# Kernel tuning notes

Hardware: AMD Instinct MI355X
Metric: run time of the kernel (lower is better)

The kernel has to match this reference:

```python
import jax, jax.numpy as jnp
import numpy as np

D = 1024
H = 16
HD = D // H
FF = 4 * D

def layer_norm(x, g, b, eps=1e-5):
    mu = jnp.mean(x, axis=-1, keepdims=True)
    var = jnp.var(x, axis=-1, keepdims=True)
    return (x - mu) * jax.lax.rsqrt(var + eps) * g + b

def setup_inputs() -> dict:
    key = jax.random.key(0)
    ks = jax.random.split(key, 8)
    s = 0.02
    return {
        "x": jax.random.normal(ks[0], (2, 2048, D), jnp.float32),
        "ln1_g": jnp.ones((D,), jnp.float32),
        "ln1_b": jnp.zeros((D,), jnp.float32),
        "w_qkv": jax.random.normal(ks[1], (3 * D, D), jnp.float32) * s,
        "b_qkv": jnp.zeros((3 * D,), jnp.float32),
        "w_proj": jax.random.normal(ks[2], (D, D), jnp.float32) * s,
        "b_proj": jnp.zeros((D,), jnp.float32),
        "ln2_g": jnp.ones((D,), jnp.float32),
        "ln2_b": jnp.zeros((D,), jnp.float32),
        "w_fc1": jax.random.normal(ks[3], (FF, D), jnp.float32) * s,
        "b_fc1": jnp.zeros((FF,), jnp.float32),
        "w_fc2": jax.random.normal(ks[4], (D, FF), jnp.float32) * s,
        "b_fc2": jnp.zeros((D,), jnp.float32),
    }

def reference(x, ln1_g, ln1_b, w_qkv, b_qkv, w_proj, b_proj,
              ln2_g, ln2_b, w_fc1, b_fc1, w_fc2, b_fc2):
    B, N, C = x.shape
    scale = HD ** -0.5
    # --- attention branch (pre-norm) ---
    h = layer_norm(x, ln1_g, ln1_b)
    qkv = h @ w_qkv.T + b_qkv                      # [B,N,3D]
    qkv = qkv.reshape(B, N, 3, H, HD).transpose(2, 0, 3, 1, 4)
    q, k, v = qkv[0], qkv[1], qkv[2]               # [B,H,N,HD]
    attn = jnp.einsum('bhnd,bhmd->bhnm', q, k) * scale
    attn = jax.nn.softmax(attn, axis=-1)
    o = jnp.einsum('bhnm,bhmd->bhnd', attn, v)     # [B,H,N,HD]
    o = o.transpose(0, 2, 1, 3).reshape(B, N, C)
    x = x + (o @ w_proj.T + b_proj)
    # --- FFN branch (pre-norm) ---
    h = layer_norm(x, ln2_g, ln2_b)
    h = jax.nn.gelu(h @ w_fc1.T + b_fc1, approximate=False)
    x = x + (h @ w_fc2.T + b_fc2)
    return x
```

## Files before the change

### kernel.cpp

```cpp
#include <hip/hip_runtime.h>

typedef __attribute__((ext_vector_type(8))) short short8;
typedef __attribute__((ext_vector_type(4))) float f32x4;

static __device__ __forceinline__ unsigned short f2bf(float f){
  unsigned u = __float_as_uint(f);
  u += 0x7FFF + ((u >> 16) & 1);
  return (unsigned short)(u >> 16);
}

static __device__ __forceinline__ f32x4 MF(short8 a, short8 b, f32x4 c){
  return __builtin_amdgcn_mfma_f32_16x16x32_bf16(a, b, c, 0, 0, 0);
}

#define GL16(g, l) __builtin_amdgcn_global_load_lds( \
    (const __attribute__((address_space(1))) void*)(g), \
    (__attribute__((address_space(3))) void*)(l), 16, 0, 0)

#define SBAR { __builtin_amdgcn_sched_barrier(0); __builtin_amdgcn_s_barrier(); __builtin_amdgcn_sched_barrier(0); }

__global__ __launch_bounds__(256) void cvt_all(
    const float* __restrict__ a0, const float* __restrict__ a1,
    const float* __restrict__ a2, const float* __restrict__ a3,
    unsigned short* __restrict__ o0, unsigned short* __restrict__ o1,
    unsigned short* __restrict__ o2, unsigned short* __restrict__ o3){
  int i = blockIdx.x * 256 + threadIdx.x;
  const float* src; unsigned short* dst; int off;
  if (i < 786432)       { src = a0; dst = o0; off = i; }
  else if (i < 1048576) { src = a1; dst = o1; off = i - 786432; }
  else if (i < 2097152) { src = a2; dst = o2; off = i - 1048576; }
  else                  { src = a3; dst = o3; off = i - 2097152; }
  float4 v = reinterpret_cast<const float4*>(src)[off];
  ushort4 o;
  o.x = f2bf(v.x); o.y = f2bf(v.y); o.z = f2bf(v.z); o.w = f2bf(v.w);
  reinterpret_cast<ushort4*>(dst)[off] = o;
}

__global__ __launch_bounds__(256) void ln_bf16(const float* __restrict__ x,
    const float* __restrict__ g, const float* __restrict__ b,
    unsigned short* __restrict__ out){
  int row = blockIdx.x, t = threadIdx.x;
  const float* xr = x + (size_t)row * 1024;
  float4 xv = reinterpret_cast<const float4*>(xr)[t];
  float s  = xv.x + xv.y + xv.z + xv.w;
  float sq = xv.x*xv.x + xv.y*xv.y + xv.z*xv.z + xv.w*xv.w;
  #pragma unroll
  for (int m = 32; m >= 1; m >>= 1){ s += __shfl_xor(s, m); sq += __shfl_xor(sq, m); }
  __shared__ float ss[4], ssq[4];
  int w = t >> 6, lane = t & 63;
  if (lane == 0){ ss[w] = s; ssq[w] = sq; }
  __syncthreads();
  s  = ss[0] + ss[1] + ss[2] + ss[3];
  sq = ssq[0] + ssq[1] + ssq[2] + ssq[3];
  float mu = s * (1.f/1024.f);
  float rs = rsqrtf(sq * (1.f/1024.f) - mu*mu + 1e-5f);
  float4 gv = reinterpret_cast<const float4*>(g)[t];
  float4 bv = reinterpret_cast<const float4*>(b)[t];
  ushort4 o;
  o.x = f2bf((xv.x - mu) * rs * gv.x + bv.x);
  o.y = f2bf((xv.y - mu) * rs * gv.y + bv.y);
  o.z = f2bf((xv.z - mu) * rs * gv.z + bv.z);
  o.w = f2bf((xv.w - mu) * rs * gv.w + bv.w);
  reinterpret_cast<ushort4*>(out + (size_t)row * 1024)[t] = o;
}

template<int EPI>
__global__ __launch_bounds__(512, 2) void gemm8p(
    const unsigned short* __restrict__ A,
    const unsigned short* __restrict__ B,
    const float* __restrict__ bias,
    void* __restrict__ C,
    int M, int N, int K)
{
  __shared__ __attribute__((aligned(16))) short As[2 * 256 * 64];
  __shared__ __attribute__((aligned(16))) short Bs[2 * 256 * 64];
  const int NT = K >> 6;
  int tid = threadIdx.x, lane = tid & 63, wave = tid >> 6;
  int wm = wave >> 2, wn = wave & 3;
  int l15 = lane & 15, hi = lane >> 4;
  int hi2 = hi ^ (((l15 >> 2) & 1) << 1);
  int bm = blockIdx.y * 256, bn = blockIdx.x * 256;
  int lr = lane >> 3;
  int sg8 = ((lane & 7) ^ ((lane >> 5) << 1)) * 8;
  int rb0 = wave * 16;

  f32x4 acc[8][4] = {};
  short8 aR[4][2], bA[2][2], bB[2][2];

  auto stage = [&](int T, int h){
    if (T >= NT) return;
    const unsigned short* src = (h < 2) ? (A + (size_t)(bm + ((h & 1) << 7)) * K)
                                        : (B + (size_t)(bn + ((h & 1) << 7)) * K);
    short* dst = ((h < 2) ? As : Bs) + ((T & 1) << 14) + ((h & 1) << 13);
    const unsigned short* s = src + (size_t)(rb0 + lr) * K + (T << 6) + sg8;
    GL16(s, dst + rb0 * 64);
    GL16(s + (size_t)8 * K, dst + (rb0 + 8) * 64);
  };
  auto LDA = [&](const short* Ab, int m, int kk){
    int R = wm * 128 + m * 16 + l15;
    return *(const short8*)(Ab + R * 64 + kk * 32 + hi2 * 8);
  };
  auto LDB = [&](const short* Bb, int n, int kk){
    int R = wn * 64 + n * 16 + l15;
    return *(const short8*)(Bb + R * 64 + kk * 32 + hi2 * 8);
  };

  stage(0, 0); stage(0, 1); stage(0, 2); stage(0, 3);
  stage(1, 0); stage(1, 1);
  asm volatile("s_waitcnt vmcnt(4)" ::: "memory");
  SBAR;

  for (int i = 0; i < (NT >> 1); ++i){
    int t0 = 2 * i, t1 = t0 + 1;
    const short* A0 = As;            const short* B0 = Bs;
    const short* A1 = As + 16384;    const short* B1 = Bs + 16384;
    #pragma unroll
    for (int m = 0; m < 4; m++){ aR[m][0] = LDA(A0, m, 0); aR[m][1] = LDA(A0, m, 1); }
    #pragma unroll
    for (int n = 0; n < 2; n++){ bA[n][0] = LDB(B0, n, 0); bA[n][1] = LDB(B0, n, 1); }
    __builtin_amdgcn_sched_barrier(0);
    stage(t1, 2);
    SBAR;
    __builtin_amdgcn_s_setprio(1);
    #pragma unroll
    for (int m = 0; m < 4; m++)
      #pragma unroll
      for (int n = 0; n < 2; n++)
        #pragma unroll
        for (int kk = 0; kk < 2; kk++) acc[m][n] = MF(aR[m][kk], bA[n][kk], acc[m][n]);
    __builtin_amdgcn_s_setprio(0);
    SBAR;
    #pragma unroll
    for (int n = 0; n < 2; n++){ bB[n][0] = LDB(B0, n + 2, 0); bB[n][1] = LDB(B0, n + 2, 1); }
    __builtin_amdgcn_sched_barrier(0);
    stage(t1, 3);
    SBAR;
    __builtin_amdgcn_s_setprio(1);
    #pragma unroll
    for (int m = 0; m < 4; m++)
      #pragma unroll
      for (int n = 0; n < 2; n++)
        #pragma unroll
        for (int kk = 0; kk < 2; kk++) acc[m][n + 2] = MF(aR[m][kk], bB[n][kk], acc[m][n + 2]);
    __builtin_amdgcn_s_setprio(0);
    SBAR;
    #pragma unroll
    for (int m = 0; m < 4; m++){ aR[m][0] = LDA(A0, m + 4, 0); aR[m][1] = LDA(A0, m + 4, 1); }
    __builtin_amdgcn_sched_barrier(0);
    stage(t0 + 2, 0);
    SBAR;
    __builtin_amdgcn_s_setprio(1);
    #pragma unroll
    for (int m = 0; m < 4; m++)
      #pragma unroll
      for (int n = 0; n < 2; n++)
        #pragma unroll
        for (int kk = 0; kk < 2; kk++) acc[m + 4][n] = MF(aR[m][kk], bA[n][kk], acc[m + 4][n]);
    __builtin_amdgcn_s_setprio(0);
    SBAR;
    stage(t0 + 2, 1);
    SBAR;
    __builtin_amdgcn_s_setprio(1);
    #pragma unroll
    for (int m = 0; m < 4; m++)
      #pragma unroll
      for (int n = 0; n < 2; n++)
        #pragma unroll
        for (int kk = 0; kk < 2; kk++) acc[m + 4][n + 2] = MF(aR[m][kk], bB[n][kk], acc[m + 4][n + 2]);
    __builtin_amdgcn_s_setprio(0);
    asm volatile("s_waitcnt vmcnt(4)" ::: "memory");
    SBAR;
    #pragma unroll
    for (int m = 0; m < 4; m++){ aR[m][0] = LDA(A1, m, 0); aR[m][1] = LDA(A1, m, 1); }
    #pragma unroll
    for (int n = 0; n < 2; n++){ bA[n][0] = LDB(B1, n, 0); bA[n][1] = LDB(B1, n, 1); }
    __builtin_amdgcn_sched_barrier(0);
    stage(t0 + 2, 2);
    SBAR;
    __builtin_amdgcn_s_setprio(1);
    #pragma unroll
    for (int m = 0; m < 4; m++)
      #pragma unroll
      for (int n = 0; n < 2; n++)
        #pragma unroll
        for (int kk = 0; kk < 2; kk++) acc[m][n] = MF(aR[m][kk], bA[n][kk], acc[m][n]);
    __builtin_amdgcn_s_setprio(0);
    SBAR;
    #pragma unroll
    for (int n = 0; n < 2; n++){ bB[n][0] = LDB(B1, n + 2, 0); bB[n][1] = LDB(B1, n + 2, 1); }
    __builtin_amdgcn_sched_barrier(0);
    stage(t0 + 2, 3);
    SBAR;
    __builtin_amdgcn_s_setprio(1);
    #pragma unroll
    for (int m = 0; m < 4; m++)
      #pragma unroll
      for (int n = 0; n < 2; n++)
        #pragma unroll
        for (int kk = 0; kk < 2; kk++) acc[m][n + 2] = MF(aR[m][kk], bB[n][kk], acc[m][n + 2]);
    __builtin_amdgcn_s_setprio(0);
    SBAR;
    #pragma unroll
    for (int m = 0; m < 4; m++){ aR[m][0] = LDA(A1, m + 4, 0); aR[m][1] = LDA(A1, m + 4, 1); }
    __builtin_amdgcn_sched_barrier(0);
    stage(t0 + 3, 0);
    SBAR;
    __builtin_amdgcn_s_setprio(1);
    #pragma unroll
    for (int m = 0; m < 4; m++)
      #pragma unroll
      for (int n = 0; n < 2; n++)
        #pragma unroll
        for (int kk = 0; kk < 2; kk++) acc[m + 4][n] = MF(aR[m][kk], bA[n][kk], acc[m + 4][n]);
    __builtin_amdgcn_s_setprio(0);
    SBAR;
    stage(t0 + 3, 1);
    SBAR;
    __builtin_amdgcn_s_setprio(1);
    #pragma unroll
    for (int m = 0; m < 4; m++)
      #pragma unroll
      for (int n = 0; n < 2; n++)
        #pragma unroll
        for (int kk = 0; kk < 2; kk++) acc[m + 4][n + 2] = MF(aR[m][kk], bB[n][kk], acc[m + 4][n + 2]);
    __builtin_amdgcn_s_setprio(0);
    asm volatile("s_waitcnt vmcnt(4)" ::: "memory");
    SBAR;
  }

  #pragma unroll
  for (int m = 0; m < 8; m++){
    int row = bm + wm * 128 + m * 16 + hi * 4;
    #pragma unroll
    for (int n = 0; n < 4; n++){
      int col = bn + wn * 64 + n * 16 + l15;
      float bv = bias[col];
      #pragma unroll
      for (int j = 0; j < 4; j++){
        float v = acc[m][n][j] + bv;
        if (EPI == 1){
          float w2 = v * v;
          float t = exp2f(v * fmaf(w2, 0.10294322f, 2.3022078f));
          float r = __builtin_amdgcn_rcpf(1.f + t);
          v = v - v * r;
        }
        ((unsigned short*)C)[(size_t)(row + j) * N + col] = f2bf(v);
      }
    }
  }
}

template<int EPI>
__global__ __launch_bounds__(512, 2) void gemm8p128(
    const unsigned short* __restrict__ A,
    const unsigned short* __restrict__ B,
    const float* __restrict__ bias,
    const float* __restrict__ resid,
    void* __restrict__ C,
    int M, int N, int K)
{
  __shared__ __attribute__((aligned(16))) short As[2][128 * 64];
  __shared__ __attribute__((aligned(16))) short Bs[2][128 * 64];
  const int NT = K >> 6;
  int tid = threadIdx.x, lane = tid & 63, wave = tid >> 6;
  int wm = wave >> 2, wn = wave & 3;
  int l15 = lane & 15, hi = lane >> 4, l7 = l15 & 7;
  int lin = blockIdx.y * 8 + blockIdx.x;
  int xcd = lin & 7, idx = lin >> 3;
  int bm = (xcd * 4 + (idx >> 3)) * 128;
  int bn = (idx & 7) * 128;
  int lr = lane >> 3;
  int sega = ((lane & 7) ^ lr) * 8;
  f32x4 acc[4][2] = {};
  short8 aR[4][2], bf0[2], bf1[2];

  auto stage = [&](int T, int h){
    if (T >= NT) return;
    const unsigned short* src = (h < 2) ? (A + (size_t)bm * K) : (B + (size_t)bn * K);
    short* dst = ((h < 2) ? &As[0][0] : &Bs[0][0]) + (T & 1) * (128 * 64);
    int row = ((h & 1) << 6) + wave * 8;
    GL16(src + (size_t)(row + lr) * K + (T << 6) + sega, dst + row * 64);
  };
  auto LDA = [&](const short* Ab, int m, int kk){
    int R = wm * 64 + m * 16 + l15;
    return *(const short8*)(Ab + R * 64 + (((kk << 2) | hi) ^ l7) * 8);
  };
  auto LDB = [&](const short* Bb, int n, int kk){
    int R = wn * 32 + n * 16 + l15;
    return *(const short8*)(Bb + R * 64 + (((kk << 2) | hi) ^ l7) * 8);
  };

  stage(0, 0); stage(0, 1); stage(0, 2); stage(0, 3);
  stage(1, 0); stage(1, 1);
  asm volatile("s_waitcnt vmcnt(2)" ::: "memory");
  SBAR;

  const short* A0 = &As[0][0]; const short* B0 = &Bs[0][0];
  const short* A1 = &As[1][0]; const short* B1 = &Bs[1][0];

  for (int i = 0; i < (NT >> 1) - 1; ++i){
    int t0 = 2 * i, t1 = t0 + 1;
    #pragma unroll
    for (int m = 0; m < 4; m++){ aR[m][0] = LDA(A0, m, 0); aR[m][1] = LDA(A0, m, 1); }
    bf0[0] = LDB(B0, 0, 0); bf0[1] = LDB(B0, 0, 1);
    __builtin_amdgcn_sched_barrier(0);
    stage(t1, 2); stage(t1, 3);
    SBAR;
    __builtin_amdgcn_s_setprio(1);
    #pragma unroll
    for (int m = 0; m < 4; m++)
      #pragma unroll
      for (int kk = 0; kk < 2; kk++) acc[m][0] = MF(aR[m][kk], bf0[kk], acc[m][0]);
    __builtin_amdgcn_s_setprio(0);
    SBAR;
    bf1[0] = LDB(B0, 1, 0); bf1[1] = LDB(B0, 1, 1);
    __builtin_amdgcn_sched_barrier(0);
    stage(t0 + 2, 0); stage(t0 + 2, 1);
    SBAR;
    __builtin_amdgcn_s_setprio(1);
    #pragma unroll
    for (int m = 0; m < 4; m++)
      #pragma unroll
      for (int kk = 0; kk < 2; kk++) acc[m][1] = MF(aR[m][kk], bf1[kk], acc[m][1]);
    __builtin_amdgcn_s_setprio(0);
    asm volatile("s_waitcnt vmcnt(2)" ::: "memory");
    SBAR;
    #pragma unroll
    for (int m = 0; m < 4; m++){ aR[m][0] = LDA(A1, m, 0); aR[m][1] = LDA(A1, m, 1); }
    bf0[0] = LDB(B1, 0, 0); bf0[1] = LDB(B1, 0, 1);
    __builtin_amdgcn_sched_barrier(0);
    stage(t0 + 2, 2); stage(t0 + 2, 3);
    SBAR;
    __builtin_amdgcn_s_setprio(1);
    #pragma unroll
    for (int m = 0; m < 4; m++)
      #pragma unroll
      for (int kk = 0; kk < 2; kk++) acc[m][0] = MF(aR[m][kk], bf0[kk], acc[m][0]);
    __builtin_amdgcn_s_setprio(0);
    SBAR;
    bf1[0] = LDB(B1, 1, 0); bf1[1] = LDB(B1, 1, 1);
    __builtin_amdgcn_sched_barrier(0);
    stage(t0 + 3, 0); stage(t0 + 3, 1);
    SBAR;
    __builtin_amdgcn_s_setprio(1);
    #pragma unroll
    for (int m = 0; m < 4; m++)
      #pragma unroll
      for (int kk = 0; kk < 2; kk++) acc[m][1] = MF(aR[m][kk], bf1[kk], acc[m][1]);
    __builtin_amdgcn_s_setprio(0);
    asm volatile("s_waitcnt vmcnt(2)" ::: "memory");
    SBAR;
  }
  {
    #pragma unroll
    for (int m = 0; m < 4; m++){ aR[m][0] = LDA(A0, m, 0); aR[m][1] = LDA(A0, m, 1); }
    bf0[0] = LDB(B0, 0, 0); bf0[1] = LDB(B0, 0, 1);
    __builtin_amdgcn_sched_barrier(0);
    int t1 = NT - 1;
    stage(t1, 2); stage(t1, 3);
    SBAR;
    __builtin_amdgcn_s_setprio(1);
    #pragma unroll
    for (int m = 0; m < 4; m++)
      #pragma unroll
      for (int kk = 0; kk < 2; kk++) acc[m][0] = MF(aR[m][kk], bf0[kk], acc[m][0]);
    __builtin_amdgcn_s_setprio(0);
    SBAR;
    bf1[0] = LDB(B0, 1, 0); bf1[1] = LDB(B0, 1, 1);
    SBAR;
    __builtin_amdgcn_s_setprio(1);
    #pragma unroll
    for (int m = 0; m < 4; m++)
      #pragma unroll
      for (int kk = 0; kk < 2; kk++) acc[m][1] = MF(aR[m][kk], bf1[kk], acc[m][1]);
    __builtin_amdgcn_s_setprio(0);
    asm volatile("s_waitcnt vmcnt(0)" ::: "memory");
    SBAR;
    #pragma unroll
    for (int m = 0; m < 4; m++){ aR[m][0] = LDA(A1, m, 0); aR[m][1] = LDA(A1, m, 1); }
    bf0[0] = LDB(B1, 0, 0); bf0[1] = LDB(B1, 0, 1);
    SBAR;
    __builtin_amdgcn_s_setprio(1);
    #pragma unroll
    for (int m = 0; m < 4; m++)
      #pragma unroll
      for (int kk = 0; kk < 2; kk++) acc[m][0] = MF(aR[m][kk], bf0[kk], acc[m][0]);
    __builtin_amdgcn_s_setprio(0);
    SBAR;
    bf1[0] = LDB(B1, 1, 0); bf1[1] = LDB(B1, 1, 1);
    __builtin_amdgcn_s_setprio(1);
    #pragma unroll
    for (int m = 0; m < 4; m++)
      #pragma unroll
      for (int kk = 0; kk < 2; kk++) acc[m][1] = MF(aR[m][kk], bf1[kk], acc[m][1]);
    __builtin_amdgcn_s_setprio(0);
  }

  #pragma unroll
  for (int m = 0; m < 4; m++){
    int row = bm + wm * 64 + m * 16 + hi * 4;
    #pragma unroll
    for (int n = 0; n < 2; n++){
      int col = bn + wn * 32 + n * 16 + l15;
      float bv = bias[col];
      #pragma unroll
      for (int j = 0; j < 4; j++){
        float v = acc[m][n][j] + bv;
        int r = row + j;
        if (EPI == 2){
          ((float*)C)[(size_t)r * N + col] = v + resid[(size_t)r * N + col];
        } else {
          ((unsigned short*)C)[(size_t)r * N + col] = f2bf(v);
        }
      }
    }
  }
}

__global__ __launch_bounds__(512) void attn_fwd(const unsigned short* __restrict__ qkv,
                                                unsigned short* __restrict__ o){
  __shared__ __attribute__((aligned(16))) short K_lds[2][64*64];
  __shared__ __attribute__((aligned(16))) short V_lds[2][64*64];
  __shared__ __attribute__((aligned(16))) short P_lds[8][16*64];
  int tid = threadIdx.x, wave = tid >> 6, lane = tid & 63;
  int l15 = lane & 15, hi = lane >> 4, l7 = l15 & 7;
  int bid = blockIdx.x;
  int swz = (bid & 7) * 64 + (bid >> 3);
  int qt = swz & 15, bh = swz >> 4;
  int b = bh >> 4, h = bh & 15;
  const unsigned short* qbase = qkv + (size_t)b * 2048 * 3072 + h * 64;
  const unsigned short* kbase = qbase + 1024;
  const unsigned short* vbase = qbase + 2048;
  int qrow = qt * 128 + wave * 16 + l15;
  short8 qf0 = *(const short8*)(qbase + (size_t)qrow * 3072 + hi * 8);
  short8 qf1 = *(const short8*)(qbase + (size_t)qrow * 3072 + 32 + hi * 8);
  #pragma unroll
  for (int j = 0; j < 8; j++){
    float q0 = __uint_as_float((unsigned)(unsigned short)qf0[j] << 16) * 0.18033688f;
    float q1 = __uint_as_float((unsigned)(unsigned short)qf1[j] << 16) * 0.18033688f;
    qf0[j] = (short)f2bf(q0);
    qf1[j] = (short)f2bf(q1);
  }
  short8 ones8;
  #pragma unroll
  for (int j = 0; j < 8; j++) ones8[j] = (short)0x3F80;
  int krow = tid >> 3, kseg = tid & 7;
  int vt = tid - 256;
  int kp = vt & 31, ds8 = (vt >> 5) & 7;
  int vcg = kp >> 2, vwi = (2 * kp) & 7;
  f32x4 accO[4] = {};
  f32x4 lacc = {};
  short* Pw = &P_lds[wave][0];

  {
    short8 kv = *(const short8*)(kbase + (size_t)krow * 3072 + kseg * 8);
    short8 vv0, vv1;
    if (vt >= 0){
      const unsigned short* vr = vbase + (size_t)(2 * kp) * 3072 + ds8 * 8;
      vv0 = *(const short8*)vr; vv1 = *(const short8*)(vr + 3072);
    }
    *(short8*)(&K_lds[0][krow * 64 + ((kseg ^ (krow & 7)) << 3)]) = kv;
    if (vt >= 0){
      unsigned* Vw = (unsigned*)&V_lds[0][0];
      #pragma unroll
      for (int j = 0; j < 8; j++){
        int d = ds8 * 8 + j;
        int sa = d * 64 + ((vcg ^ (d & 7)) << 3) + vwi;
        Vw[sa >> 1] = (unsigned)(unsigned short)vv0[j] | ((unsigned)(unsigned short)vv1[j] << 16);
      }
    }
    __syncthreads();
  }

  for (int t = 0; t < 32; t++){
    int cur = t & 1;
    const short* Kc = &K_lds[cur][0];
    const short* Vc = &V_lds[cur][0];
    short8 kv, vv0, vv1;
    if (t < 31){
      int kt = (t + 1) * 64;
      kv = *(const short8*)(kbase + (size_t)(kt + krow) * 3072 + kseg * 8);
      if (vt >= 0){
        const unsigned short* vr = vbase + (size_t)(kt + 2 * kp) * 3072 + ds8 * 8;
        vv0 = *(const short8*)vr; vv1 = *(const short8*)(vr + 3072);
      }
    }
    f32x4 sacc[4];
    __builtin_amdgcn_s_setprio(1);
    #pragma unroll
    for (int kb = 0; kb < 4; kb++){
      f32x4 s = {};
      short8 ka = *(const short8*)(Kc + (kb * 16 + l15) * 64 + ((hi ^ l7) << 3));
      s = __builtin_amdgcn_mfma_f32_16x16x32_bf16(ka, qf0, s, 0, 0, 0);
      short8 kb_ = *(const short8*)(Kc + (kb * 16 + l15) * 64 + (((4 + hi) ^ l7) << 3));
      s = __builtin_amdgcn_mfma_f32_16x16x32_bf16(kb_, qf1, s, 0, 0, 0);
      sacc[kb] = s;
    }
    __builtin_amdgcn_s_setprio(0);
    unsigned pu[8];
    #pragma unroll
    for (int kb = 0; kb < 4; kb++){
      unsigned u0 = (unsigned)(int)fmaf(sacc[kb][0], 128.f, 16248.6f);
      unsigned u1 = (unsigned)(int)fmaf(sacc[kb][1], 128.f, 16248.6f);
      unsigned u2 = (unsigned)(int)fmaf(sacc[kb][2], 128.f, 16248.6f);
      unsigned u3 = (unsigned)(int)fmaf(sacc[kb][3], 128.f, 16248.6f);
      pu[kb * 2]     = u0 | (u1 << 16);
      pu[kb * 2 + 1] = u2 | (u3 << 16);
    }
    #pragma unroll
    for (int kb = 0; kb < 4; kb++){
      int sa = l15 * 64 + ((((kb << 1) | (hi >> 1)) ^ l7) << 3) + ((hi & 1) << 2);
      *(uint2*)(Pw + sa) = make_uint2(pu[kb * 2], pu[kb * 2 + 1]);
    }
    __builtin_amdgcn_s_setprio(1);
    #pragma unroll
    for (int kb2 = 0; kb2 < 2; kb2++){
      short8 pf = *(const short8*)(Pw + l15 * 64 + ((((kb2 << 2) | hi) ^ l7) << 3));
      #pragma unroll
      for (int db = 0; db < 4; db++){
        short8 vf = *(const short8*)(Vc + (db * 16 + l15) * 64 + ((((kb2 << 2) | hi) ^ l7) << 3));
        accO[db] = __builtin_amdgcn_mfma_f32_16x16x32_bf16(vf, pf, accO[db], 0, 0, 0);
      }
      lacc = __builtin_amdgcn_mfma_f32_16x16x32_bf16(ones8, pf, lacc, 0, 0, 0);
    }
    __builtin_amdgcn_s_setprio(0);
    if (t < 31){
      int nxt = cur ^ 1;
      *(short8*)(&K_lds[nxt][krow * 64 + ((kseg ^ (krow & 7)) << 3)]) = kv;
      if (vt >= 0){
        unsigned* Vw = (unsigned*)&V_lds[nxt][0];
        #pragma unroll
        for (int j = 0; j < 8; j++){
          int d = ds8 * 8 + j;
          int sa = d * 64 + ((vcg ^ (d & 7)) << 3) + vwi;
          Vw[sa >> 1] = (unsigned)(unsigned short)vv0[j] | ((unsigned)(unsigned short)vv1[j] << 16);
        }
      }
      __syncthreads();
    }
  }
  float inv = 1.f / lacc[0];
  unsigned short* ob = o + (size_t)(b * 2048 + qt * 128 + wave * 16 + l15) * 1024 + h * 64;
  #pragma unroll
  for (int db = 0; db < 4; db++){
    ushort4 w;
    w.x = f2bf(accO[db][0] * inv);
    w.y = f2bf(accO[db][1] * inv);
    w.z = f2bf(accO[db][2] * inv);
    w.w = f2bf(accO[db][3] * inv);
    *(ushort4*)(ob + db * 16 + hi * 4) = w;
  }
}

extern "C" void kernel_launch(void* const* d_in, const int* in_sizes, int n_in,
                              void* d_out, int out_size, void* d_ws, size_t ws_size,
                              hipStream_t stream){
  const float* x      = (const float*)d_in[0];
  const float* ln1_g  = (const float*)d_in[1];
  const float* ln1_b  = (const float*)d_in[2];
  const float* w_qkv  = (const float*)d_in[3];
  const float* b_qkv  = (const float*)d_in[4];
  const float* w_proj = (const float*)d_in[5];
  const float* b_proj = (const float*)d_in[6];
  const float* ln2_g  = (const float*)d_in[7];
  const float* ln2_b  = (const float*)d_in[8];
  const float* w_fc1  = (const float*)d_in[9];
  const float* b_fc1  = (const float*)d_in[10];
  const float* w_fc2  = (const float*)d_in[11];
  const float* b_fc2  = (const float*)d_in[12];
  float* out = (float*)d_out;
  char* ws = (char*)d_ws;
  const size_t MB = 1024 * 1024;
  unsigned short* h     = (unsigned short*)(ws);
  unsigned short* qkv   = (unsigned short*)(ws + 8*MB);
  unsigned short* ob    = (unsigned short*)(ws + 32*MB);
  float*          x1    = (float*)(ws + 40*MB);
  unsigned short* f     = (unsigned short*)(ws + 56*MB);
  unsigned short* wqkvb = (unsigned short*)(ws + 88*MB);
  unsigned short* wprojb= (unsigned short*)(ws + 94*MB);
  unsigned short* wfc1b = (unsigned short*)(ws + 96*MB);
  unsigned short* wfc2b = (unsigned short*)(ws + 104*MB);

  cvt_all<<<12288, 256, 0, stream>>>(w_qkv, w_proj, w_fc1, w_fc2,
                                     wqkvb, wprojb, wfc1b, wfc2b);

  ln_bf16<<<4096, 256, 0, stream>>>(x, ln1_g, ln1_b, h);
  gemm8p<0><<<dim3(12, 16), 512, 0, stream>>>(h, wqkvb, b_qkv, qkv, 4096, 3072, 1024);
  attn_fwd<<<512, 512, 0, stream>>>(qkv, ob);
  gemm8p128<2><<<dim3(8, 32), 512, 0, stream>>>(ob, wprojb, b_proj, x, x1, 4096, 1024, 1024);
  ln_bf16<<<4096, 256, 0, stream>>>(x1, ln2_g, ln2_b, h);
  gemm8p<1><<<dim3(16, 16), 512, 0, stream>>>(h, wfc1b, b_fc1, f, 4096, 4096, 1024);
  gemm8p128<2><<<dim3(8, 32), 512, 0, stream>>>(f, wfc2b, b_fc2, x1, out, 4096, 1024, 4096);
}
```

Baseline: 221.8 us.

## Split K and V tile loading across wave halves and simplify GEMM block mapping

In the attention kernel, K-tile loading now goes to the first 256 threads, two 16-byte loads each, and V loading stays with the other 256 threads. Previously all 512 threads loaded K and half also loaded V. This balances per-thread global load and LDS store work and removes duplicated register pressure. The GEMM's XCD-aware block swizzle is also replaced with a plain row-major block mapping, which may change L2 locality across XCDs.

```diff
diff --git a/kernel.cpp b/kernel.cpp
--- a/kernel.cpp
+++ b/kernel.cpp
@@ -266,9 +266,8 @@
   int wm = wave >> 2, wn = wave & 3;
   int l15 = lane & 15, hi = lane >> 4, l7 = l15 & 7;
   int lin = blockIdx.y * 8 + blockIdx.x;
-  int xcd = lin & 7, idx = lin >> 3;
-  int bm = (xcd * 4 + (idx >> 3)) * 128;
-  int bn = (idx & 7) * 128;
+  int bn = (lin & 7) * 128;
+  int bm = (lin >> 3) * 128;
   int lr = lane >> 3;
   int sega = ((lane & 7) ^ lr) * 8;
   f32x4 acc[4][2] = {};
@@ -444,31 +443,45 @@
   short8 ones8;
   #pragma unroll
   for (int j = 0; j < 8; j++) ones8[j] = (short)0x3F80;
-  int krow = tid >> 3, kseg = tid & 7;
   int vt = tid - 256;
+  int ki0 = tid * 2, ki1 = ki0 + 1;
+  int kr0 = ki0 >> 3, ks0 = ki0 & 7;
+  int kr1 = ki1 >> 3, ks1 = ki1 & 7;
   int kp = vt & 31, ds8 = (vt >> 5) & 7;
   int vcg = kp >> 2, vwi = (2 * kp) & 7;
   f32x4 accO[4] = {};
   f32x4 lacc = {};
   short* Pw = &P_lds[wave][0];
 
-  {
-    short8 kv = *(const short8*)(kbase + (size_t)krow * 3072 + kseg * 8);
-    short8 vv0, vv1;
-    if (vt >= 0){
-      const unsigned short* vr = vbase + (size_t)(2 * kp) * 3072 + ds8 * 8;
-      vv0 = *(const short8*)vr; vv1 = *(const short8*)(vr + 3072);
-    }
-    *(short8*)(&K_lds[0][krow * 64 + ((kseg ^ (krow & 7)) << 3)]) = kv;
-    if (vt >= 0){
-      unsigned* Vw = (unsigned*)&V_lds[0][0];
+  auto kv_load = [&](int kt, short8& s0, short8& s1){
+    if (vt < 0){
+      s0 = *(const short8*)(kbase + (size_t)(kt + kr0) * 3072 + ks0 * 8);
+      s1 = *(const short8*)(kbase + (size_t)(kt + kr1) * 3072 + ks1 * 8);
+    } else {
+      const unsigned short* vr = vbase + (size_t)(kt + 2 * kp) * 3072 + ds8 * 8;
+      s0 = *(const short8*)vr;
+      s1 = *(const short8*)(vr + 3072);
+    }
+  };
+  auto kv_store = [&](int buf, short8 s0, short8 s1){
+    if (vt < 0){
+      *(short8*)(&K_lds[buf][kr0 * 64 + ((ks0 ^ (kr0 & 7)) << 3)]) = s0;
+      *(short8*)(&K_lds[buf][kr1 * 64 + ((ks1 ^ (kr1 & 7)) << 3)]) = s1;
+    } else {
+      unsigned* Vw = (unsigned*)&V_lds[buf][0];
       #pragma unroll
       for (int j = 0; j < 8; j++){
         int d = ds8 * 8 + j;
         int sa = d * 64 + ((vcg ^ (d & 7)) << 3) + vwi;
-        Vw[sa >> 1] = (unsigned)(unsigned short)vv0[j] | ((unsigned)(unsigned short)vv1[j] << 16);
+        Vw[sa >> 1] = (unsigned)(unsigned short)s0[j] | ((unsigned)(unsigned short)s1[j] << 16);
       }
     }
+  };
+
+  {
+    short8 s0, s1;
+    kv_load(0, s0, s1);
+    kv_store(0, s0, s1);
     __syncthreads();
   }
 
@@ -476,15 +489,8 @@
     int cur = t & 1;
     const short* Kc = &K_lds[cur][0];
     const short* Vc = &V_lds[cur][0];
-    short8 kv, vv0, vv1;
-    if (t < 31){
-      int kt = (t + 1) * 64;
-      kv = *(const short8*)(kbase + (size_t)(kt + krow) * 3072 + kseg * 8);
-      if (vt >= 0){
-        const unsigned short* vr = vbase + (size_t)(kt + 2 * kp) * 3072 + ds8 * 8;
-        vv0 = *(const short8*)vr; vv1 = *(const short8*)(vr + 3072);
-      }
-    }
+    short8 s0, s1;
+    if (t < 31) kv_load((t + 1) * 64, s0, s1);
     f32x4 sacc[4];
     __builtin_amdgcn_s_setprio(1);
     #pragma unroll
@@ -525,17 +531,7 @@
     }
     __builtin_amdgcn_s_setprio(0);
     if (t < 31){
-      int nxt = cur ^ 1;
-      *(short8*)(&K_lds[nxt][krow * 64 + ((kseg ^ (krow & 7)) << 3)]) = kv;
-      if (vt >= 0){
-        unsigned* Vw = (unsigned*)&V_lds[nxt][0];
-        #pragma unroll
-        for (int j = 0; j < 8; j++){
-          int d = ds8 * 8 + j;
-          int sa = d * 64 + ((vcg ^ (d & 7)) << 3) + vwi;
-          Vw[sa >> 1] = (unsigned)(unsigned short)vv0[j] | ((unsigned)(unsigned short)vv1[j] << 16);
-        }
-      }
+      kv_store(cur ^ 1, s0, s1);
       __syncthreads();
     }
   }
```

Result: slower. 238.5 us (+7.6%).
